# Kernel optimization log

Measured on AMD Instinct MI355X. Metric: run time of the kernel, lower is better.

The kernel has to match this reference:

```python
import jax, jax.numpy as jnp
import numpy as np
from jax import lax

B, L, R = 128, 256, 36
D_TXT, D_IMG, D_SOC = 768, 2048, 10
EPS = 0.05 ** 2        # geomloss blur=0.05, p=2 -> epsilon = blur^p
N_ITERS = 20           # fixed log-domain Sinkhorn iterations
GAMMA = 0.01


def _pcost(x, y):
    # x: [B,n,d], y: [B,m,d] -> C_ij = ||x_i - y_j||^2 / 2 (geomloss p=2 cost)
    xx = jnp.sum(x * x, -1)[:, :, None]
    yy = jnp.sum(y * y, -1)[:, None, :]
    xy = jnp.einsum('bnd,bmd->bnm', x, y)
    return 0.5 * (xx + yy - 2.0 * xy)


def _sinkhorn_cost(C, loga, logb, eps, n_iters):
    # Log-domain Sinkhorn; masked points carry loga/logb = -inf (zero weight).
    f = jnp.zeros(loga.shape, C.dtype)
    g = jnp.zeros(logb.shape, C.dtype)

    def body(fg, _):
        f, g = fg
        g = -eps * jax.nn.logsumexp(loga[:, :, None] + (f[:, :, None] - C) / eps, axis=1)
        f = -eps * jax.nn.logsumexp(logb[:, None, :] + (g[:, None, :] - C) / eps, axis=2)
        return (f, g), None

    (f, g), _ = lax.scan(body, (f, g), None, length=n_iters)
    a = jnp.exp(loga)  # exp(-inf) = 0 for masked entries
    b = jnp.exp(logb)
    return jnp.sum(a * f, -1) + jnp.sum(b * g, -1)  # <a,f> + <b,g>


def _forward(txt_global, txt_region, img_global, img_region, social, attn_mask,
             W_stat, b_stat, W_gt, b_gt, W_gi, b_gi, W_rt, b_rt, W_ri, b_ri,
             W_m1, b_m1, W_m2, b_m2):
    relu = jax.nn.relu
    soc = relu(social @ W_stat + b_stat)                            # [B,100]
    tg = relu(jnp.concatenate([txt_global, soc], axis=1) @ W_gt + b_gt)  # [B,200]
    ig = relu(img_global @ W_gi + b_gi)                              # [B,200]
    h = relu((tg + ig) @ W_m1 + b_m1)
    mix_pred = h @ W_m2 + b_m2                                       # [B,2]

    tr = relu(txt_region @ W_rt + b_rt)                              # [B,L,50]
    ir = relu(img_region @ W_ri + b_ri)                              # [B,R,50]

    Bn, _, _ = tr.shape
    Rn = ir.shape[1]
    mask = attn_mask > 0
    n_words = jnp.sum(attn_mask, axis=-1).astype(tr.dtype)          # [B]
    loga = jnp.where(mask, -jnp.log(n_words)[:, None], -jnp.inf)    # uniform over valid tokens
    logb = jnp.full((Bn, Rn), -jnp.log(float(Rn)), tr.dtype)        # uniform over regions

    # Debiased Sinkhorn divergence (geomloss SamplesLoss default debias=True):
    Sxy = _sinkhorn_cost(_pcost(tr, ir), loga, logb, EPS, N_ITERS)
    Sxx = _sinkhorn_cost(_pcost(tr, tr), loga, loga, EPS, N_ITERS)
    Syy = _sinkhorn_cost(_pcost(ir, ir), logb, logb, EPS, N_ITERS)
    w_dis = Sxy - 0.5 * (Sxx + Syy)                                  # [B]

    w_pred = jnp.stack([1.0 - GAMMA * w_dis, GAMMA * w_dis], axis=1)  # [B,2]
    logit = jax.nn.softmax(jnp.maximum(mix_pred, w_pred), axis=1)
    return logit


def setup_inputs() -> dict:
    key = jax.random.key(0)
    ks = jax.random.split(key, 24)
    init = lambda k, s: (jax.random.normal(k, s) * 0.02).astype(jnp.float32)
    lengths = jax.random.randint(ks[0], (B,), 16, L + 1)             # ragged lengths
    attn_mask = (jnp.arange(L)[None, :] < lengths[:, None]).astype(jnp.int32)
    return {
        'txt_global': jax.random.normal(ks[1], (B, D_TXT), jnp.float32),
        'txt_region': jax.random.normal(ks[2], (B, L, D_TXT), jnp.float32),
        'img_global': jax.random.normal(ks[3], (B, D_IMG), jnp.float32),
        'img_region': jax.random.normal(ks[4], (B, R, D_IMG), jnp.float32),
        'social': jax.random.normal(ks[5], (B, D_SOC), jnp.float32),
        'attn_mask': attn_mask,
        'W_stat': init(ks[6], (D_SOC, 100)), 'b_stat': jnp.zeros((100,), jnp.float32),
        'W_gt': init(ks[7], (868, 200)), 'b_gt': jnp.zeros((200,), jnp.float32),
        'W_gi': init(ks[8], (D_IMG, 200)), 'b_gi': jnp.zeros((200,), jnp.float32),
        'W_rt': init(ks[9], (D_TXT, 50)), 'b_rt': jnp.zeros((50,), jnp.float32),
        'W_ri': init(ks[10], (D_IMG, 50)), 'b_ri': jnp.zeros((50,), jnp.float32),
        'W_m1': init(ks[11], (200, 100)), 'b_m1': jnp.zeros((100,), jnp.float32),
        'W_m2': init(ks[12], (100, 2)), 'b_m2': jnp.zeros((2,), jnp.float32),
    }


def reference(txt_global, txt_region, img_global, img_region, social, attn_mask,
              W_stat, b_stat, W_gt, b_gt, W_gi, b_gi, W_rt, b_rt, W_ri, b_ri,
              W_m1, b_m1, W_m2, b_m2):
    return _forward(txt_global, txt_region, img_global, img_region, social, attn_mask,
                    W_stat, b_stat, W_gt, b_gt, W_gi, b_gi, W_rt, b_rt, W_ri, b_ri,
                    W_m1, b_m1, W_m2, b_m2)
```

## Files before the change

kernel.cpp:

```cpp
#include <hip/hip_runtime.h>

typedef float  f32x4 __attribute__((ext_vector_type(4)));
typedef short  s16x8 __attribute__((ext_vector_type(8)));

#define EPS_LN2      0.0017328679513998632f
#define INV_EPS_LN2  577.0780163555852f
#define LOG2_36      5.169925001442312f

__device__ __forceinline__ short f2bf(float x) {
  unsigned int u; __builtin_memcpy(&u, &x, 4);
  u = (u + 0x7FFFu + ((u >> 16) & 1u)) >> 16;
  return (short)u;
}

__global__ __launch_bounds__(256) void k_prep(
    const float* __restrict__ W_rt, const float* __restrict__ W_ri,
    short* __restrict__ frt, short* __restrict__ fri,
    const float* __restrict__ txt, const float* __restrict__ img,
    const float* __restrict__ social,
    const float* __restrict__ W_stat, const float* __restrict__ b_stat,
    const float* __restrict__ W_gt, const float* __restrict__ W_gi,
    float* __restrict__ pre) {
  __shared__ float sA[32][128];
  int bid = blockIdx.x;
  if (bid < 88) {
    int slot = bid * 256 + threadIdx.x;
    const float* W; short* dst; int f;
    if (slot < 6144) { W = W_rt; dst = frt; f = slot; }
    else             { W = W_ri; dst = fri; f = slot - 6144; }
    int k32 = f >> 8, rem = f & 255, ct = rem >> 6, l = rem & 63;
    int col = ct * 16 + (l & 15);
    int k0  = k32 * 32 + (l >> 4) * 8;
    s16x8 p;
#pragma unroll
    for (int c = 0; c < 8; ++c) {
      float v = (col < 50) ? W[(k0 + c) * 50 + col] : 0.f;
      p[c] = f2bf(v);
    }
    *(s16x8*)(dst + (long)f * 8) = p;
    return;
  }
  int gb = bid - 88;
  int job = gb >> 4, rb = (gb >> 2) & 3, cb = gb & 3;
  int t = threadIdx.x, r0 = rb * 32;
  const float* W; int k0, klen;
  if (job < 6)       { k0 = job * 128;       klen = 128; W = W_gt; }
  else if (job == 6) { k0 = 0;               klen = 100; W = W_gt + 768 * 200; }
  else               { k0 = (job - 7) * 128; klen = 128; W = W_gi; }
  if (job == 6) {
    for (int idx = t; idx < 4096; idx += 256) {
      int r = idx >> 7, k = idx & 127;
      float v = 0.f;
      if (k < 100) {
        v = b_stat[k];
#pragma unroll
        for (int u = 0; u < 10; ++u) v += social[(r0 + r) * 10 + u] * W_stat[u * 100 + k];
        v = fmaxf(v, 0.f);
      }
      sA[r][k] = v;
    }
  } else {
    const float* A = (job < 6) ? txt : img;
    int K_A = (job < 6) ? 768 : 2048;
    for (int idx = t; idx < 4096; idx += 256) {
      int r = idx >> 7, k = idx & 127;
      sA[r][k] = A[(r0 + r) * K_A + k0 + k];
    }
  }
  __syncthreads();
  int c = cb * 64 + (t & 63), rg = t >> 6;
  if (c < 200) {
    float acc[8];
#pragma unroll
    for (int i = 0; i < 8; ++i) acc[i] = 0.f;
    for (int k4 = 0; k4 < klen; k4 += 4) {
      float w0 = W[(k0 + k4    ) * 200 + c];
      float w1 = W[(k0 + k4 + 1) * 200 + c];
      float w2 = W[(k0 + k4 + 2) * 200 + c];
      float w3 = W[(k0 + k4 + 3) * 200 + c];
#pragma unroll
      for (int i = 0; i < 8; ++i) {
        f32x4 a = *(const f32x4*)&sA[rg * 8 + i][k4];
        acc[i] += a[0]*w0 + a[1]*w1 + a[2]*w2 + a[3]*w3;
      }
    }
    float* dst = pre + (long)job * 25600;
#pragma unroll
    for (int i = 0; i < 8; ++i)
      dst[(r0 + rg * 8 + i) * 200 + c] = acc[i];
  }
}

template<int K32>
__device__ __forceinline__ void proj_body(const float* __restrict__ A,
                                          const short* __restrict__ Bf,
                                          const float* __restrict__ bias,
                                          float* __restrict__ out, int bid,
                                          float* __restrict__ red) {
  constexpr int KH = K32 / 2;
  constexpr int D  = 3;
  int wave = threadIdx.x >> 6, lane = threadIdx.x & 63;
  int rg = wave >> 1, ks = wave & 1;
  int rl = lane & 15, q = lane >> 4;
  int row0 = bid * 32 + rg * 16;
  const int K = K32 * 32;
  const float* ar = A + (long)(row0 + rl) * K + ks * (KH * 32) + q * 8;
  const s16x8* bp = (const s16x8*)Bf + ks * (KH * 256) + lane;

  f32x4 pa0[D], pa1[D];
  s16x8 pb0[D], pb1[D], pb2[D], pb3[D];
#pragma unroll
  for (int d = 0; d < D; ++d) {
    pa0[d] = *(const f32x4*)(ar + d * 32);
    pa1[d] = *(const f32x4*)(ar + d * 32 + 4);
    const s16x8* p = bp + d * 256;
    pb0[d] = p[0]; pb1[d] = p[64]; pb2[d] = p[128]; pb3[d] = p[192];
  }
  f32x4 acc[4];
#pragma unroll
  for (int ct = 0; ct < 4; ++ct) acc[ct] = (f32x4){0.f, 0.f, 0.f, 0.f};

#pragma unroll
  for (int k32 = 0; k32 < KH; ++k32) {
    int slot = k32 % D;
    s16x8 af;
    af[0]=f2bf(pa0[slot][0]); af[1]=f2bf(pa0[slot][1]);
    af[2]=f2bf(pa0[slot][2]); af[3]=f2bf(pa0[slot][3]);
    af[4]=f2bf(pa1[slot][0]); af[5]=f2bf(pa1[slot][1]);
    af[6]=f2bf(pa1[slot][2]); af[7]=f2bf(pa1[slot][3]);
    acc[0] = __builtin_amdgcn_mfma_f32_16x16x32_bf16(af, pb0[slot], acc[0], 0, 0, 0);
    acc[1] = __builtin_amdgcn_mfma_f32_16x16x32_bf16(af, pb1[slot], acc[1], 0, 0, 0);
    acc[2] = __builtin_amdgcn_mfma_f32_16x16x32_bf16(af, pb2[slot], acc[2], 0, 0, 0);
    acc[3] = __builtin_amdgcn_mfma_f32_16x16x32_bf16(af, pb3[slot], acc[3], 0, 0, 0);
    if (k32 + D < KH) {
      pa0[slot] = *(const f32x4*)(ar + (k32 + D) * 32);
      pa1[slot] = *(const f32x4*)(ar + (k32 + D) * 32 + 4);
      const s16x8* p = bp + (k32 + D) * 256;
      pb0[slot] = p[0]; pb1[slot] = p[64]; pb2[slot] = p[128]; pb3[slot] = p[192];
    }
  }

  float* rb = red + rg * 1024;
  if (ks == 1) {
#pragma unroll
    for (int ct = 0; ct < 4; ++ct)
      *(f32x4*)(rb + lane * 16 + ct * 4) = acc[ct];
  }
  __syncthreads();
  if (ks == 0) {
#pragma unroll
    for (int ct = 0; ct < 4; ++ct) {
      f32x4 o = *(const f32x4*)(rb + lane * 16 + ct * 4);
      int col = ct * 16 + rl;
      float bv = (col < 50) ? bias[col] : 0.f;
#pragma unroll
      for (int r = 0; r < 4; ++r) {
        int grow = row0 + q * 4 + r;
        float v = fmaxf(acc[ct][r] + o[r] + bv, 0.f);
        out[(long)grow * 64 + col] = (col < 50) ? v : 0.f;
      }
    }
  }
}

__device__ __forceinline__ void mix_body(
    int r, const float* __restrict__ pre,
    const float* __restrict__ b_gt, const float* __restrict__ b_gi,
    const float* __restrict__ W_m1, const float* __restrict__ b_m1,
    const float* __restrict__ W_m2, const float* __restrict__ b_m2,
    float* __restrict__ mix, float* smem) {
  float* sm = smem;
  float* sh = smem + 200;
  int t = threadIdx.x;
  if (t < 200) {
    float s1 = b_gt[t], s2 = b_gi[t];
#pragma unroll
    for (int j = 0; j < 7; ++j)  s1 += pre[(long)j * 25600 + r * 200 + t];
#pragma unroll
    for (int j = 7; j < 23; ++j) s2 += pre[(long)j * 25600 + r * 200 + t];
    sm[t] = fmaxf(s1, 0.f) + fmaxf(s2, 0.f);
  }
  __syncthreads();
  if (t < 100) {
    float a = b_m1[t];
#pragma unroll 4
    for (int k = 0; k < 200; ++k) a += sm[k] * W_m1[k * 100 + t];
    sh[t] = fmaxf(a, 0.f);
  }
  __syncthreads();
  if (t < 2) {
    float a = b_m2[t];
    for (int k = 0; k < 100; ++k) a += sh[k] * W_m2[k * 2 + t];
    mix[r * 2 + t] = a;
  }
}

__global__ __launch_bounds__(256)
__attribute__((amdgpu_waves_per_eu(4, 4)))
void k_pm(
    const float* __restrict__ txt_region, const short* __restrict__ frt,
    const float* __restrict__ b_rt, float* __restrict__ tr,
    const float* __restrict__ img_region, const short* __restrict__ fri,
    const float* __restrict__ b_ri, float* __restrict__ ir,
    const float* __restrict__ pre,
    const float* __restrict__ b_gt, const float* __restrict__ b_gi,
    const float* __restrict__ W_m1, const float* __restrict__ b_m1,
    const float* __restrict__ W_m2, const float* __restrict__ b_m2,
    float* __restrict__ mix) {
  __shared__ __align__(16) float smem[2048];
  int bid = blockIdx.x;
  if (bid < 144)       proj_body<64>(img_region, fri, b_ri, ir, bid, smem);
  else if (bid < 1168) proj_body<24>(txt_region, frt, b_rt, tr, bid - 144, smem);
  else                 mix_body(bid - 1168, pre, b_gt, b_gi, W_m1, b_m1, W_m2, b_m2, mix, smem);
}

#define SK_SMEM 50736

__global__ __launch_bounds__(1024)
__attribute__((amdgpu_waves_per_eu(4, 4)))
void k_sink(
    const float* __restrict__ tr, const float* __restrict__ ir,
    const int* __restrict__ amask, float* __restrict__ Cxx,
    float* __restrict__ Sxy, float* __restrict__ Sxx, float* __restrict__ Syy) {
  __shared__ __align__(16) char smem[SK_SMEM];
  int role = blockIdx.x >> 7;
  int b    = blockIdx.x & 127;
  int tid  = threadIdx.x;

  if (role == 0) {
    short* Xf    = (short*)smem;
    float* norms = (float*)(smem + 32768);
    float* sA    = (float*)(smem + 33792);
    float* sF    = (float*)(smem + 34816);
    float* sG    = (float*)(smem + 35840);
    float* sPm   = (float*)(smem + 36864);
    int*   nsh   = (int*)  (smem + 40960);
    if (tid < 64) {
      int c = 0;
      for (int i = tid; i < 256; i += 64) c += amask[b * 256 + i];
#pragma unroll
      for (int o = 1; o < 64; o <<= 1) c += __shfl_xor(c, o);
      if (tid == 0) *nsh = c;
    }
    const float* Xg = tr + (long)b * 256 * 64;
    for (int slot = tid; slot < 2048; slot += 1024) {
      int t = slot >> 7, k32 = (slot >> 6) & 1, l = slot & 63;
      int row = t * 16 + (l & 15), k0 = k32 * 32 + (l >> 4) * 8;
      const float* src = Xg + row * 64 + k0;
      f32x4 a0 = *(const f32x4*)src, a1 = *(const f32x4*)(src + 4);
      s16x8 p;
      p[0]=f2bf(a0[0]); p[1]=f2bf(a0[1]); p[2]=f2bf(a0[2]); p[3]=f2bf(a0[3]);
      p[4]=f2bf(a1[0]); p[5]=f2bf(a1[1]); p[6]=f2bf(a1[2]); p[7]=f2bf(a1[3]);
      *(s16x8*)(Xf + slot * 8) = p;
    }
    __syncthreads();
    int n = *nsh;
    int wv = tid >> 6, lane = tid & 63, q = lane >> 4;
    f32x4 acc[16];
#pragma unroll
    for (int ct = 0; ct < 16; ++ct) acc[ct] = (f32x4){0.f, 0.f, 0.f, 0.f};
    s16x8 afr0 = *(const s16x8*)(Xf + ((wv * 2 + 0) * 64 + lane) * 8);
    s16x8 afr1 = *(const s16x8*)(Xf + ((wv * 2 + 1) * 64 + lane) * 8);
#pragma unroll
    for (int ct = 0; ct < 16; ++ct) {
      s16x8 b0 = *(const s16x8*)(Xf + ((ct * 2 + 0) * 64 + lane) * 8);
      s16x8 b1 = *(const s16x8*)(Xf + ((ct * 2 + 1) * 64 + lane) * 8);
      acc[ct] = __builtin_amdgcn_mfma_f32_16x16x32_bf16(afr0, b0, acc[ct], 0, 0, 0);
      acc[ct] = __builtin_amdgcn_mfma_f32_16x16x32_bf16(afr1, b1, acc[ct], 0, 0, 0);
    }
#pragma unroll
    for (int r = 0; r < 4; ++r) {
      int m_ = q * 4 + r;
      if ((lane & 15) == m_) norms[wv * 16 + m_] = acc[wv][r];
    }
    __syncthreads();
    float* Cwb = Cxx + (long)b * 65536;
    if (wv * 16 < n) {
#pragma unroll
      for (int ct = 0; ct < 16; ++ct) {
        int gj = ct * 16 + (lane & 15);
        float nj = norms[gj];
#pragma unroll
        for (int r = 0; r < 4; ++r) {
          int gi = wv * 16 + q * 4 + r;
          Cwb[gi * 256 + gj] = (acc[ct][r] - 0.5f * (norms[gi] + nj)) * INV_EPS_LN2;
        }
      }
    }
    __syncthreads();
    int kk = tid >> 8, j = tid & 255, i0 = kk * 64;
    int iend = n - i0; if (iend > 64) iend = 64;
    float Creg[64];
    if (j < n) {
#pragma unroll
      for (int ch = 0; ch < 4; ++ch) {
        if (ch * 16 < iend) {
#pragma unroll
          for (int u = 0; u < 16; ++u)
            Creg[ch * 16 + u] = Cwb[(i0 + ch * 16 + u) * 256 + j];
        }
      }
    }
    float log2n = log2f((float)n);
    if (tid < 256) { sF[tid] = 0.f; sA[tid] = (tid < n) ? -log2n : -1e30f; }
    __syncthreads();
    const float* ap = sA + i0;
    for (int h = 0; h < 40; ++h) {
      float m = -1e30f;
      if (j < n) {
#pragma unroll
        for (int ch = 0; ch < 4; ++ch) {
          if (ch * 16 < iend) {
            const float* app = ap + ch * 16;
            f32x4 A0 = *(const f32x4*)(app);
            f32x4 A1 = *(const f32x4*)(app + 4);
            f32x4 A2 = *(const f32x4*)(app + 8);
            f32x4 A3 = *(const f32x4*)(app + 12);
            float x0 = A0[0]+Creg[ch*16+0],  x1 = A0[1]+Creg[ch*16+1];
            float x2 = A0[2]+Creg[ch*16+2],  x3 = A0[3]+Creg[ch*16+3];
            float x4 = A1[0]+Creg[ch*16+4],  x5 = A1[1]+Creg[ch*16+5];
            float x6 = A1[2]+Creg[ch*16+6],  x7 = A1[3]+Creg[ch*16+7];
            float x8 = A2[0]+Creg[ch*16+8],  x9 = A2[1]+Creg[ch*16+9];
            float xa = A2[2]+Creg[ch*16+10], xb = A2[3]+Creg[ch*16+11];
            float xc = A3[0]+Creg[ch*16+12], xd = A3[1]+Creg[ch*16+13];
            float xe = A3[2]+Creg[ch*16+14], xf = A3[3]+Creg[ch*16+15];
            float y0 = fmaxf(fmaxf(x0, x1), x2);
            float y1 = fmaxf(fmaxf(x3, x4), x5);
            float y2 = fmaxf(fmaxf(x6, x7), x8);
            float y3 = fmaxf(fmaxf(x9, xa), xb);
            float y4 = fmaxf(fmaxf(xc, xd), xe);
            float z0 = fmaxf(fmaxf(y0, y1), y2);
            float z1 = fmaxf(fmaxf(y3, y4), xf);
            m = fmaxf(fmaxf(m, z0), z1);
          }
        }
      }
      sPm[kk * 256 + j] = m;
      __syncthreads();
      if (tid < 256) {
        float m4 = fmaxf(fmaxf(sPm[tid], sPm[256 + tid]),
                         fmaxf(sPm[512 + tid], sPm[768 + tid]));
        if (tid < n) {
          ((h & 1) ? sF : sG)[tid] = -EPS_LN2 * m4;
          sA[tid] = -log2n - m4;
        }
      }
      __syncthreads();
    }
    if (tid < 64) {
      float a = 0.f;
      for (int i = tid; i < n; i += 64) a += sF[i] + sG[i];
#pragma unroll
      for (int o = 1; o < 64; o <<= 1) a += __shfl_xor(a, o);
      if (tid == 0) Sxx[b] = a / n;
    }
  } else if (role == 1) {
    float* Ys  = (float*)smem;
    float* Cs  = (float*)(smem + 9216);
    float* nx  = (float*)(smem + 47104);
    float* ny  = (float*)(smem + 48128);
    float* sA  = (float*)(smem + 48288);
    float* sB  = (float*)(smem + 49376);
    float* sF  = (float*)(smem + 49536);
    float* sG  = (float*)(smem + 50560);
    int*   nsh = (int*)  (smem + 50720);
    if (tid < 64) {
      int c = 0;
      for (int i = tid; i < 256; i += 64) c += amask[b * 256 + i];
#pragma unroll
      for (int o = 1; o < 64; o <<= 1) c += __shfl_xor(c, o);
      if (tid == 0) *nsh = c;
    }
    const float* Xg = tr + (long)b * 256 * 64;
    const float* Yg = ir + (long)b * 36 * 64;
    for (int idx = tid; idx < 576; idx += 1024) {
      int row = idx >> 4, q4 = idx & 15;
      *(f32x4*)(Ys + row * 64 + q4 * 4) = *(const f32x4*)(Yg + row * 64 + q4 * 4);
    }
    __syncthreads();
    int n = *nsh;
    if (tid < 256) {
      float a = 0.f;
#pragma unroll
      for (int q4 = 0; q4 < 13; ++q4) {
        f32x4 v = *(const f32x4*)(Xg + tid * 64 + q4 * 4);
        a += v[0]*v[0] + v[1]*v[1] + v[2]*v[2] + v[3]*v[3];
      }
      nx[tid] = a;
    } else if (tid < 292) {
      int jj = tid - 256; float a = 0.f;
#pragma unroll
      for (int q4 = 0; q4 < 13; ++q4) {
        f32x4 v = *(const f32x4*)(Ys + jj * 64 + q4 * 4);
        a += v[0]*v[0] + v[1]*v[1] + v[2]*v[2] + v[3]*v[3];
      }
      ny[jj] = a;
    }
    __syncthreads();
    if (tid < 1008) {
      int ii = tid / 36, jj = tid - ii * 36;
      f32x4 yr[13];
#pragma unroll
      for (int q4 = 0; q4 < 13; ++q4) yr[q4] = *(const f32x4*)(Ys + jj * 64 + q4 * 4);
      float nyj = ny[jj];
      for (int i = ii; i < 256; i += 28) {
        float d = 0.f;
#pragma unroll
        for (int q4 = 0; q4 < 13; ++q4) {
          f32x4 xv = *(const f32x4*)(Xg + i * 64 + q4 * 4);
          d += xv[0]*yr[q4][0] + xv[1]*yr[q4][1] + xv[2]*yr[q4][2] + xv[3]*yr[q4][3];
        }
        Cs[i * 37 + jj] = (d - 0.5f * (nx[i] + nyj)) * INV_EPS_LN2;
      }
    }
    __syncthreads();
    int jg = tid >> 4, kg = tid & 15;
    float Cg[16];
    if (jg < 36) {
#pragma unroll
      for (int t = 0; t < 16; ++t) Cg[t] = Cs[(kg * 16 + t) * 37 + jg];
    }
    int fi = tid >> 2, kf = tid & 3;
    float Cf[9];
#pragma unroll
    for (int t = 0; t < 9; ++t) {
      int jj2 = kf * 9 + t;
      Cf[t] = (jj2 < 36) ? Cs[fi * 37 + jj2] : 0.f;
    }
    float log2n = log2f((float)n);
    if (tid < 256) { sF[tid] = 0.f; sA[tid + (tid >> 4)] = -log2n; }
    __syncthreads();
    const float* agp = sA + kg * 17;
    int gend = n - kg * 16; if (gend > 16) gend = 16;
    for (int it = 0; it < 20; ++it) {
      float gm = -1e30f;
      if (jg < 36) {
#pragma unroll
        for (int t = 0; t < 16; ++t)
          if (t < gend) gm = fmaxf(gm, agp[t] + Cg[t]);
        gm = fmaxf(gm, __shfl_xor(gm, 1)); gm = fmaxf(gm, __shfl_xor(gm, 2));
        gm = fmaxf(gm, __shfl_xor(gm, 4)); gm = fmaxf(gm, __shfl_xor(gm, 8));
      }
      __syncthreads();
      if (jg < 36 && kg == 0) {
        sG[jg] = -EPS_LN2 * gm;
        sB[jg] = -LOG2_36 - gm;
      }
      __syncthreads();
      float fm = -1e30f;
#pragma unroll
      for (int t = 0; t < 9; ++t) {
        int jj2 = kf * 9 + t;
        if (jj2 < 36) fm = fmaxf(fm, sB[jj2] + Cf[t]);
      }
      fm = fmaxf(fm, __shfl_xor(fm, 1)); fm = fmaxf(fm, __shfl_xor(fm, 2));
      __syncthreads();
      if (kf == 0 && fi < n) {
        sF[fi] = -EPS_LN2 * fm;
        sA[fi + (fi >> 4)] = -log2n - fm;
      }
      __syncthreads();
    }
    if (tid < 64) {
      float a = 0.f;
      for (int i = tid; i < n; i += 64) a += sF[i];
      float g = (tid < 36) ? sG[tid] : 0.f;
#pragma unroll
      for (int o = 1; o < 64; o <<= 1) { a += __shfl_xor(a, o); g += __shfl_xor(g, o); }
      if (tid == 0) Sxy[b] = a / n + g / 36.f;
    }
  } else {
    float* Ys = (float*)smem;
    float* Cs = (float*)(smem + 9216);
    float* ny = (float*)(smem + 48128);
    float* sA = (float*)(smem + 48288);
    float* sF = (float*)(smem + 49536);
    float* sG = (float*)(smem + 50560);
    const float* Yg = ir + (long)b * 36 * 64;
    for (int idx = tid; idx < 576; idx += 1024) {
      int row = idx >> 4, q4 = idx & 15;
      *(f32x4*)(Ys + row * 64 + q4 * 4) = *(const f32x4*)(Yg + row * 64 + q4 * 4);
    }
    __syncthreads();
    if (tid < 36) {
      float a = 0.f;
#pragma unroll
      for (int q4 = 0; q4 < 13; ++q4) {
        f32x4 v = *(const f32x4*)(Ys + tid * 64 + q4 * 4);
        a += v[0]*v[0] + v[1]*v[1] + v[2]*v[2] + v[3]*v[3];
      }
      ny[tid] = a;
    }
    __syncthreads();
    if (tid < 1008) {
      int ii = tid / 36, jj = tid - ii * 36;
      f32x4 yr[13];
#pragma unroll
      for (int q4 = 0; q4 < 13; ++q4) yr[q4] = *(const f32x4*)(Ys + jj * 64 + q4 * 4);
      float nyj = ny[jj];
      for (int i = ii; i < 36; i += 28) {
        float d = 0.f;
#pragma unroll
        for (int q4 = 0; q4 < 13; ++q4) {
          f32x4 xv = *(const f32x4*)(Ys + i * 64 + q4 * 4);
          d += xv[0]*yr[q4][0] + xv[1]*yr[q4][1] + xv[2]*yr[q4][2] + xv[3]*yr[q4][3];
        }
        Cs[i * 37 + jj] = (d - 0.5f * (ny[i] + nyj)) * INV_EPS_LN2;
      }
    }
    __syncthreads();
    int j = tid >> 2, kk = tid & 3;
    float Creg[9];
    if (j < 36) {
#pragma unroll
      for (int t = 0; t < 9; ++t) {
        int i2 = kk * 9 + t;
        Creg[t] = (i2 < 36) ? Cs[i2 * 37 + j] : 0.f;
      }
    }
    if (tid < 36) { sF[tid] = 0.f; sA[tid] = -LOG2_36; }
    __syncthreads();
    for (int h = 0; h < 40; ++h) {
      float m = -1e30f;
      if (j < 36) {
#pragma unroll
        for (int t = 0; t < 9; ++t) {
          int i2 = kk * 9 + t;
          if (i2 < 36) m = fmaxf(m, sA[i2] + Creg[t]);
        }
        m = fmaxf(m, __shfl_xor(m, 1)); m = fmaxf(m, __shfl_xor(m, 2));
      }
      __syncthreads();
      if (j < 36 && kk == 0) {
        ((h & 1) ? sF : sG)[j] = -EPS_LN2 * m;
        sA[j] = -LOG2_36 - m;
      }
      __syncthreads();
    }
    if (tid < 64) {
      float a = (tid < 36) ? sF[tid] + sG[tid] : 0.f;
#pragma unroll
      for (int o = 1; o < 64; o <<= 1) a += __shfl_xor(a, o);
      if (tid == 0) Syy[b] = a / 36.f;
    }
  }
}

__global__ void k_final(const float* __restrict__ mix, const float* __restrict__ sxy,
                        const float* __restrict__ sxx, const float* __restrict__ syy,
                        float* __restrict__ out) {
  int b = blockIdx.x * 64 + threadIdx.x;
  if (b < 128) {
    float w  = sxy[b] - 0.5f * (sxx[b] + syy[b]);
    float x0 = fmaxf(mix[b * 2 + 0], 1.0f - 0.01f * w);
    float x1 = fmaxf(mix[b * 2 + 1], 0.01f * w);
    float mx = fmaxf(x0, x1);
    float e0 = expf(x0 - mx), e1 = expf(x1 - mx);
    float inv = 1.f / (e0 + e1);
    out[b * 2 + 0] = e0 * inv;
    out[b * 2 + 1] = e1 * inv;
  }
}

extern "C" void kernel_launch(void* const* d_in, const int* in_sizes, int n_in,
                              void* d_out, int out_size, void* d_ws, size_t ws_size,
                              hipStream_t stream) {
  const float* txt_global = (const float*)d_in[0];
  const float* txt_region = (const float*)d_in[1];
  const float* img_global = (const float*)d_in[2];
  const float* img_region = (const float*)d_in[3];
  const float* social     = (const float*)d_in[4];
  const int*   attn_mask  = (const int*)  d_in[5];
  const float* W_stat = (const float*)d_in[6];  const float* b_stat = (const float*)d_in[7];
  const float* W_gt   = (const float*)d_in[8];  const float* b_gt   = (const float*)d_in[9];
  const float* W_gi   = (const float*)d_in[10]; const float* b_gi   = (const float*)d_in[11];
  const float* W_rt   = (const float*)d_in[12]; const float* b_rt   = (const float*)d_in[13];
  const float* W_ri   = (const float*)d_in[14]; const float* b_ri   = (const float*)d_in[15];
  const float* W_m1   = (const float*)d_in[16]; const float* b_m1   = (const float*)d_in[17];
  const float* W_m2   = (const float*)d_in[18]; const float* b_m2   = (const float*)d_in[19];

  float* ws = (float*)d_ws;
  float* ws_mix = ws;
  float* ws_sxy = ws + 256;
  float* ws_sxx = ws + 384;
  float* ws_syy = ws + 512;
  short* ws_frt = (short*)(ws + 1024);
  short* ws_fri = (short*)(ws + 25600);
  float* ws_tr  = ws + 131072;
  float* ws_ir  = ws + 2228224;
  float* ws_cxx = ws + 2523136;
  float* ws_pre = ws_cxx;

  k_prep<<<456, 256, 0, stream>>>(W_rt, W_ri, ws_frt, ws_fri,
                                  txt_global, img_global, social,
                                  W_stat, b_stat, W_gt, W_gi, ws_pre);
  k_pm<<<1296, 256, 0, stream>>>(txt_region, ws_frt, b_rt, ws_tr,
                                 img_region, ws_fri, b_ri, ws_ir,
                                 ws_pre, b_gt, b_gi,
                                 W_m1, b_m1, W_m2, b_m2, ws_mix);
  k_sink<<<384, 1024, 0, stream>>>(ws_tr, ws_ir, attn_mask, ws_cxx,
                                   ws_sxy, ws_sxx, ws_syy);
  k_final<<<2, 64, 0, stream>>>(ws_mix, ws_sxy, ws_sxx, ws_syy, (float*)d_out);
}
```

Measured before the change: 322.2 us.

## Keep self-cost matrix in LDS as fp16 with packed-half Sinkhorn, stage projection via LDS

The text-text Sinkhorn block now writes its cost matrix to a swizzled fp16 transposed LDS buffer instead of round-tripping it through global memory and holding it in 64 registers. The max-reduction uses packed f16 add/max instructions. The region projection kernel switches from register prefetch to double-buffered global_load_lds staging with a swizzled layout, and the waves_per_eu caps are removed. fp16 costs and potentials reduce accuracy, and the larger LDS footprint lowers occupancy.

```diff
diff --git a/kernel.cpp b/kernel.cpp
--- a/kernel.cpp
+++ b/kernel.cpp
@@ -1,7 +1,8 @@
 #include <hip/hip_runtime.h>
 
-typedef float  f32x4 __attribute__((ext_vector_type(4)));
-typedef short  s16x8 __attribute__((ext_vector_type(8)));
+typedef float        f32x4 __attribute__((ext_vector_type(4)));
+typedef short        s16x8 __attribute__((ext_vector_type(8)));
+typedef unsigned int u32x4 __attribute__((ext_vector_type(4)));
 
 #define EPS_LN2      0.0017328679513998632f
 #define INV_EPS_LN2  577.0780163555852f
@@ -12,6 +13,17 @@
   u = (u + 0x7FFFu + ((u >> 16) & 1u)) >> 16;
   return (short)u;
 }
+
+__device__ __forceinline__ unsigned short f2h(float x) {
+  return __builtin_bit_cast(unsigned short, (_Float16)x);
+}
+__device__ __forceinline__ float h2f(unsigned short h) {
+  return (float)__builtin_bit_cast(_Float16, h);
+}
+
+#define GLOAD16(g, l) __builtin_amdgcn_global_load_lds( \
+    (const __attribute__((address_space(1))) void*)(g), \
+    (__attribute__((address_space(3))) void*)(l), 16, 0, 0)
 
 __global__ __launch_bounds__(256) void k_prep(
     const float* __restrict__ W_rt, const float* __restrict__ W_ri,
@@ -96,61 +108,73 @@
                                           const short* __restrict__ Bf,
                                           const float* __restrict__ bias,
                                           float* __restrict__ out, int bid,
-                                          float* __restrict__ red) {
+                                          char* smem) {
   constexpr int KH = K32 / 2;
-  constexpr int D  = 3;
   int wave = threadIdx.x >> 6, lane = threadIdx.x & 63;
   int rg = wave >> 1, ks = wave & 1;
-  int rl = lane & 15, q = lane >> 4;
+  int rl = lane & 15, q = lane >> 4, r7 = rl & 7;
   int row0 = bid * 32 + rg * 16;
   const int K = K32 * 32;
-  const float* ar = A + (long)(row0 + rl) * K + ks * (KH * 32) + q * 8;
-  const s16x8* bp = (const s16x8*)Bf + ks * (KH * 256) + lane;
-
-  f32x4 pa0[D], pa1[D];
-  s16x8 pb0[D], pb1[D], pb2[D], pb3[D];
-#pragma unroll
-  for (int d = 0; d < D; ++d) {
-    pa0[d] = *(const f32x4*)(ar + d * 32);
-    pa1[d] = *(const f32x4*)(ar + d * 32 + 4);
-    const s16x8* p = bp + d * 256;
-    pb0[d] = p[0]; pb1[d] = p[64]; pb2[d] = p[128]; pb3[d] = p[192];
-  }
+  char* wbuf = smem + wave * 12288;
+
+  int ra = lane >> 3, pa = lane & 7;
+  int fsw = (pa ^ ra) * 4;
+  const float* asrc0 = A + (long)(row0 + ra)     * K + ks * (KH * 32) + fsw;
+  const float* asrc1 = A + (long)(row0 + 8 + ra) * K + ks * (KH * 32) + fsw;
+  const short* bsrc  = Bf + (long)ks * (KH * 2048) + lane * 8;
+
+#define PSTAGE(KK, ST) { \
+    char* ad = wbuf + (ST) * 6144; \
+    GLOAD16(asrc0 + (KK) * 32, ad); \
+    GLOAD16(asrc1 + (KK) * 32, ad + 1024); \
+    char* bd = ad + 2048; \
+    const short* bs = bsrc + (KK) * 2048; \
+    GLOAD16(bs,        bd); \
+    GLOAD16(bs + 512,  bd + 1024); \
+    GLOAD16(bs + 1024, bd + 2048); \
+    GLOAD16(bs + 1536, bd + 3072); \
+  }
+
   f32x4 acc[4];
 #pragma unroll
   for (int ct = 0; ct < 4; ++ct) acc[ct] = (f32x4){0.f, 0.f, 0.f, 0.f};
 
-#pragma unroll
-  for (int k32 = 0; k32 < KH; ++k32) {
-    int slot = k32 % D;
+  PSTAGE(0, 0);
+#pragma unroll
+  for (int k = 0; k < KH; ++k) {
+    if (k + 1 < KH) {
+      PSTAGE(k + 1, (k + 1) & 1);
+      asm volatile("s_waitcnt vmcnt(6)" ::: "memory");
+    } else {
+      asm volatile("s_waitcnt vmcnt(0)" ::: "memory");
+    }
+    __builtin_amdgcn_sched_barrier(0);
+    const char* ab = wbuf + (k & 1) * 6144;
+    f32x4 a0 = *(const f32x4*)(ab + rl * 128 + (((q * 2)     ^ r7) << 4));
+    f32x4 a1 = *(const f32x4*)(ab + rl * 128 + (((q * 2 + 1) ^ r7) << 4));
+    const char* bb = ab + 2048;
     s16x8 af;
-    af[0]=f2bf(pa0[slot][0]); af[1]=f2bf(pa0[slot][1]);
-    af[2]=f2bf(pa0[slot][2]); af[3]=f2bf(pa0[slot][3]);
-    af[4]=f2bf(pa1[slot][0]); af[5]=f2bf(pa1[slot][1]);
-    af[6]=f2bf(pa1[slot][2]); af[7]=f2bf(pa1[slot][3]);
-    acc[0] = __builtin_amdgcn_mfma_f32_16x16x32_bf16(af, pb0[slot], acc[0], 0, 0, 0);
-    acc[1] = __builtin_amdgcn_mfma_f32_16x16x32_bf16(af, pb1[slot], acc[1], 0, 0, 0);
-    acc[2] = __builtin_amdgcn_mfma_f32_16x16x32_bf16(af, pb2[slot], acc[2], 0, 0, 0);
-    acc[3] = __builtin_amdgcn_mfma_f32_16x16x32_bf16(af, pb3[slot], acc[3], 0, 0, 0);
-    if (k32 + D < KH) {
-      pa0[slot] = *(const f32x4*)(ar + (k32 + D) * 32);
-      pa1[slot] = *(const f32x4*)(ar + (k32 + D) * 32 + 4);
-      const s16x8* p = bp + (k32 + D) * 256;
-      pb0[slot] = p[0]; pb1[slot] = p[64]; pb2[slot] = p[128]; pb3[slot] = p[192];
-    }
-  }
-
-  float* rb = red + rg * 1024;
+    af[0]=f2bf(a0[0]); af[1]=f2bf(a0[1]); af[2]=f2bf(a0[2]); af[3]=f2bf(a0[3]);
+    af[4]=f2bf(a1[0]); af[5]=f2bf(a1[1]); af[6]=f2bf(a1[2]); af[7]=f2bf(a1[3]);
+#pragma unroll
+    for (int ct = 0; ct < 4; ++ct) {
+      s16x8 bfr = *(const s16x8*)(bb + ct * 1024 + lane * 16);
+      acc[ct] = __builtin_amdgcn_mfma_f32_16x16x32_bf16(af, bfr, acc[ct], 0, 0, 0);
+    }
+  }
+#undef PSTAGE
+
   if (ks == 1) {
 #pragma unroll
     for (int ct = 0; ct < 4; ++ct)
-      *(f32x4*)(rb + lane * 16 + ct * 4) = acc[ct];
+      *(f32x4*)(wbuf + ct * 1024 + lane * 16) = acc[ct];
   }
   __syncthreads();
   if (ks == 0) {
+    const char* pb = smem + (wave + 1) * 12288;
 #pragma unroll
     for (int ct = 0; ct < 4; ++ct) {
-      f32x4 o = *(const f32x4*)(rb + lane * 16 + ct * 4);
+      f32x4 o = *(const f32x4*)(pb + ct * 1024 + lane * 16);
       int col = ct * 16 + rl;
       float bv = (col < 50) ? bias[col] : 0.f;
 #pragma unroll
@@ -196,7 +220,6 @@
 }
 
 __global__ __launch_bounds__(256)
-__attribute__((amdgpu_waves_per_eu(4, 4)))
 void k_pm(
     const float* __restrict__ txt_region, const short* __restrict__ frt,
     const float* __restrict__ b_rt, float* __restrict__ tr,
@@ -207,20 +230,19 @@
     const float* __restrict__ W_m1, const float* __restrict__ b_m1,
     const float* __restrict__ W_m2, const float* __restrict__ b_m2,
     float* __restrict__ mix) {
-  __shared__ __align__(16) float smem[2048];
+  __shared__ __align__(16) char smem[49152];
   int bid = blockIdx.x;
   if (bid < 144)       proj_body<64>(img_region, fri, b_ri, ir, bid, smem);
   else if (bid < 1168) proj_body<24>(txt_region, frt, b_rt, tr, bid - 144, smem);
-  else                 mix_body(bid - 1168, pre, b_gt, b_gi, W_m1, b_m1, W_m2, b_m2, mix, smem);
-}
-
-#define SK_SMEM 50736
+  else                 mix_body(bid - 1168, pre, b_gt, b_gi, W_m1, b_m1, W_m2, b_m2, mix, (float*)smem);
+}
+
+#define SK_SMEM 139264
 
 __global__ __launch_bounds__(1024)
-__attribute__((amdgpu_waves_per_eu(4, 4)))
 void k_sink(
     const float* __restrict__ tr, const float* __restrict__ ir,
-    const int* __restrict__ amask, float* __restrict__ Cxx,
+    const int* __restrict__ amask,
     float* __restrict__ Sxy, float* __restrict__ Sxx, float* __restrict__ Syy) {
   __shared__ __align__(16) char smem[SK_SMEM];
   int role = blockIdx.x >> 7;
@@ -228,13 +250,14 @@
   int tid  = threadIdx.x;
 
   if (role == 0) {
-    short* Xf    = (short*)smem;
-    float* norms = (float*)(smem + 32768);
-    float* sA    = (float*)(smem + 33792);
-    float* sF    = (float*)(smem + 34816);
-    float* sG    = (float*)(smem + 35840);
-    float* sPm   = (float*)(smem + 36864);
-    int*   nsh   = (int*)  (smem + 40960);
+    short*     Xf    = (short*)smem;
+    char*      CT    = smem;
+    float*     norms = (float*)(smem + 131072);
+    float*     sPm   = (float*)(smem + 132096);
+    float*     sF    = (float*)(smem + 136192);
+    float*     sG    = (float*)(smem + 137216);
+    _Float16*  sAh   = (_Float16*)(smem + 138240);
+    int*       nsh   = (int*)  (smem + 138784);
     if (tid < 64) {
       int c = 0;
       for (int i = tid; i < 256; i += 64) c += amask[b * 256 + i];
@@ -274,75 +297,59 @@
       if ((lane & 15) == m_) norms[wv * 16 + m_] = acc[wv][r];
     }
     __syncthreads();
-    float* Cwb = Cxx + (long)b * 65536;
-    if (wv * 16 < n) {
-#pragma unroll
-      for (int ct = 0; ct < 16; ++ct) {
-        int gj = ct * 16 + (lane & 15);
-        float nj = norms[gj];
-#pragma unroll
-        for (int r = 0; r < 4; ++r) {
-          int gi = wv * 16 + q * 4 + r;
-          Cwb[gi * 256 + gj] = (acc[ct][r] - 0.5f * (norms[gi] + nj)) * INV_EPS_LN2;
-        }
-      }
+    int i0w = wv * 16 + q * 4;
+    float ni0 = norms[i0w], ni1 = norms[i0w + 1];
+    float ni2 = norms[i0w + 2], ni3 = norms[i0w + 3];
+#pragma unroll
+    for (int ct = 0; ct < 16; ++ct) {
+      int j = ct * 16 + (lane & 15);
+      float nj = norms[j];
+      float v0 = (acc[ct][0] - 0.5f * (ni0 + nj)) * INV_EPS_LN2;
+      float v1 = (acc[ct][1] - 0.5f * (ni1 + nj)) * INV_EPS_LN2;
+      float v2 = (acc[ct][2] - 0.5f * (ni2 + nj)) * INV_EPS_LN2;
+      float v3 = (acc[ct][3] - 0.5f * (ni3 + nj)) * INV_EPS_LN2;
+      char* p = CT + (((j << 9) + (i0w << 1)) ^ ((j & 7) << 4));
+      unsigned p01 = (unsigned)f2h(v0) | ((unsigned)f2h(v1) << 16);
+      unsigned p23 = (unsigned)f2h(v2) | ((unsigned)f2h(v3) << 16);
+      *(unsigned*)(p)     = p01;
+      *(unsigned*)(p + 4) = p23;
+    }
+    float log2n = log2f((float)n);
+    if (tid < 256) {
+      sF[tid] = 0.f;
+      sAh[tid] = (tid < n) ? (_Float16)(-log2n) : (_Float16)(-65504.f);
     }
     __syncthreads();
     int kk = tid >> 8, j = tid & 255, i0 = kk * 64;
-    int iend = n - i0; if (iend > 64) iend = 64;
-    float Creg[64];
-    if (j < n) {
-#pragma unroll
-      for (int ch = 0; ch < 4; ++ch) {
-        if (ch * 16 < iend) {
-#pragma unroll
-          for (int u = 0; u < 16; ++u)
-            Creg[ch * 16 + u] = Cwb[(i0 + ch * 16 + u) * 256 + j];
-        }
-      }
-    }
-    float log2n = log2f((float)n);
-    if (tid < 256) { sF[tid] = 0.f; sA[tid] = (tid < n) ? -log2n : -1e30f; }
-    __syncthreads();
-    const float* ap = sA + i0;
+    unsigned base = (unsigned)((j << 9) + (i0 << 1));
+    unsigned sw   = (unsigned)((j & 7) << 4);
+    const unsigned* ah2 = (const unsigned*)(sAh) + kk * 32;
     for (int h = 0; h < 40; ++h) {
-      float m = -1e30f;
-      if (j < n) {
-#pragma unroll
-        for (int ch = 0; ch < 4; ++ch) {
-          if (ch * 16 < iend) {
-            const float* app = ap + ch * 16;
-            f32x4 A0 = *(const f32x4*)(app);
-            f32x4 A1 = *(const f32x4*)(app + 4);
-            f32x4 A2 = *(const f32x4*)(app + 8);
-            f32x4 A3 = *(const f32x4*)(app + 12);
-            float x0 = A0[0]+Creg[ch*16+0],  x1 = A0[1]+Creg[ch*16+1];
-            float x2 = A0[2]+Creg[ch*16+2],  x3 = A0[3]+Creg[ch*16+3];
-            float x4 = A1[0]+Creg[ch*16+4],  x5 = A1[1]+Creg[ch*16+5];
-            float x6 = A1[2]+Creg[ch*16+6],  x7 = A1[3]+Creg[ch*16+7];
-            float x8 = A2[0]+Creg[ch*16+8],  x9 = A2[1]+Creg[ch*16+9];
-            float xa = A2[2]+Creg[ch*16+10], xb = A2[3]+Creg[ch*16+11];
-            float xc = A3[0]+Creg[ch*16+12], xd = A3[1]+Creg[ch*16+13];
-            float xe = A3[2]+Creg[ch*16+14], xf = A3[3]+Creg[ch*16+15];
-            float y0 = fmaxf(fmaxf(x0, x1), x2);
-            float y1 = fmaxf(fmaxf(x3, x4), x5);
-            float y2 = fmaxf(fmaxf(x6, x7), x8);
-            float y3 = fmaxf(fmaxf(x9, xa), xb);
-            float y4 = fmaxf(fmaxf(xc, xd), xe);
-            float z0 = fmaxf(fmaxf(y0, y1), y2);
-            float z1 = fmaxf(fmaxf(y3, y4), xf);
-            m = fmaxf(fmaxf(m, z0), z1);
-          }
-        }
-      }
-      sPm[kk * 256 + j] = m;
+      unsigned mm = 0xFBFFFBFFu;
+#pragma unroll
+      for (int s = 0; s < 8; ++s) {
+        u32x4 v = *(const u32x4*)(CT + ((base + (s << 4)) ^ sw));
+        unsigned a0 = ah2[s * 4 + 0], a1 = ah2[s * 4 + 1];
+        unsigned a2 = ah2[s * 4 + 2], a3 = ah2[s * 4 + 3];
+        unsigned t0, t1, t2, t3;
+        asm("v_pk_add_f16 %0, %1, %2" : "=v"(t0) : "v"(v[0]), "v"(a0));
+        asm("v_pk_add_f16 %0, %1, %2" : "=v"(t1) : "v"(v[1]), "v"(a1));
+        asm("v_pk_add_f16 %0, %1, %2" : "=v"(t2) : "v"(v[2]), "v"(a2));
+        asm("v_pk_add_f16 %0, %1, %2" : "=v"(t3) : "v"(v[3]), "v"(a3));
+        asm("v_pk_max_f16 %0, %0, %1" : "+v"(mm) : "v"(t0));
+        asm("v_pk_max_f16 %0, %0, %1" : "+v"(mm) : "v"(t1));
+        asm("v_pk_max_f16 %0, %0, %1" : "+v"(mm) : "v"(t2));
+        asm("v_pk_max_f16 %0, %0, %1" : "+v"(mm) : "v"(t3));
+      }
+      sPm[kk * 256 + j] = fmaxf(h2f((unsigned short)(mm & 0xFFFFu)),
+                                h2f((unsigned short)(mm >> 16)));
       __syncthreads();
       if (tid < 256) {
         float m4 = fmaxf(fmaxf(sPm[tid], sPm[256 + tid]),
                          fmaxf(sPm[512 + tid], sPm[768 + tid]));
         if (tid < n) {
           ((h & 1) ? sF : sG)[tid] = -EPS_LN2 * m4;
-          sA[tid] = -log2n - m4;
+          sAh[tid] = (_Float16)(-log2n - m4);
         }
       }
       __syncthreads();
@@ -588,8 +595,7 @@
   short* ws_fri = (short*)(ws + 25600);
   float* ws_tr  = ws + 131072;
   float* ws_ir  = ws + 2228224;
-  float* ws_cxx = ws + 2523136;
-  float* ws_pre = ws_cxx;
+  float* ws_pre = ws + 2523136;
 
   k_prep<<<456, 256, 0, stream>>>(W_rt, W_ri, ws_frt, ws_fri,
                                   txt_global, img_global, social,
@@ -598,7 +604,7 @@
                                  img_region, ws_fri, b_ri, ws_ir,
                                  ws_pre, b_gt, b_gi,
                                  W_m1, b_m1, W_m2, b_m2, ws_mix);
-  k_sink<<<384, 1024, 0, stream>>>(ws_tr, ws_ir, attn_mask, ws_cxx,
+  k_sink<<<384, 1024, 0, stream>>>(ws_tr, ws_ir, attn_mask,
                                    ws_sxy, ws_sxx, ws_syy);
   k_final<<<2, 64, 0, stream>>>(ws_mix, ws_sxy, ws_sxx, ws_syy, (float*)d_out);
 }
```

Measured after the change: 326.4 us. Within noise of the previous version (+1.3%).
